# Kernel tuning notes

Hardware: AMD Instinct MI355X
Metric: run time of the kernel (lower is better)

The kernel has to match this reference:

```python
import jax, jax.numpy as jnp
import numpy as np

DIM = 768      # d_model
D_INNER = 768  # int(ssm_ratio * dim)
KK = 16        # K (scan groups)
CD = 48        # Cdim per group (hardcoded self.C)
NS = 16        # d_state
BATCH, SEQ = 8, 4096


def setup_inputs() -> dict:
    key = jax.random.key(0)
    ks = jax.random.split(key, 12)
    s_in = (2.0 / (DIM + 2 * D_INNER)) ** 0.5   # ~xavier
    s_out = (2.0 / (D_INNER + DIM)) ** 0.5
    return {
        "x": jax.random.normal(ks[0], (BATCH, SEQ, DIM), jnp.float32),
        "in_proj_w": jax.random.normal(ks[1], (2 * D_INNER, DIM), jnp.float32) * s_in,
        "in_proj_b": jnp.zeros((2 * D_INNER,), jnp.float32),
        "conv_w": jax.random.normal(ks[2], (D_INNER, 1, 3, 3), jnp.float32) * 0.2,
        "conv_b": jnp.zeros((D_INNER,), jnp.float32),
        "out_proj_w": jax.random.normal(ks[3], (DIM, D_INNER), jnp.float32) * s_out,
        "out_proj_b": jnp.zeros((DIM,), jnp.float32),
        "A_logs": jax.random.normal(ks[4], (KK * CD, NS), jnp.float32) * 0.1,
        "delta": jax.random.normal(ks[5], (BATCH, KK * CD, SEQ), jnp.float32),
        "B_t": jax.random.normal(ks[6], (BATCH, KK, NS, SEQ), jnp.float32),
        "C_t": jax.random.normal(ks[7], (BATCH, KK, NS, SEQ), jnp.float32),
        "delta_bias": jax.random.normal(ks[8], (KK * CD,), jnp.float32),
    }


def reference(x, in_proj_w, in_proj_b, conv_w, conv_b, out_proj_w, out_proj_b,
              A_logs, delta, B_t, C_t, delta_bias):
    # in_proj + chunk; z = silu(z) in the original is dead code (never used)
    h = x @ in_proj_w.T + in_proj_b                      # (B,N,2*D)
    u = h[..., :D_INNER]                                  # (B,N,D)
    # depthwise 3x3 conv on a (B,D,N,1) map (width-1 input, pad 1)
    u = u.transpose(0, 2, 1)[..., None]                   # (B,D,N,1)
    u = jax.lax.conv_general_dilated(
        u, conv_w, window_strides=(1, 1), padding=((1, 1), (1, 1)),
        dimension_numbers=("NCHW", "OIHW", "NCHW"),
        feature_group_count=D_INNER)
    u = jax.nn.silu(u[..., 0] + conv_b[None, :, None])    # (B,D,N)

    # selective_scan_torch math (note: NOT a true recurrence in the source):
    #   delta <- softplus(delta + delta_bias)
    #   y[b,d,l] = delta^2 * u * sum_n A[d,n] * B[b,k(d),n,l] * C[b,k(d),n,l]
    d = jax.nn.softplus(delta + delta_bias[None, :, None])  # (B,D,L)
    A = A_logs.reshape(KK, CD, NS)
    s = jnp.einsum("kcn,bknl->bkcl", A, B_t * C_t)           # (B,K,Cd,L)
    s = s.reshape(u.shape[0], D_INNER, u.shape[2])           # (B,D,L)
    y = d * d * u * s                                        # (B,D,L)

    out = y.transpose(0, 2, 1) @ out_proj_w.T + out_proj_b   # (B,N,dim)
    return out
```

## Files before the change

kernel.cpp:

```cpp
#include <hip/hip_runtime.h>
#include <math.h>

#define B_  8
#define S_  4096
#define D_  768
#define K_  16
#define C_  48
#define N_  16
#define M_  (B_*S_)

typedef float  f32x4  __attribute__((ext_vector_type(4)));
typedef __bf16 bf16x8 __attribute__((ext_vector_type(8)));

__device__ __forceinline__ ushort f2bf(float f) {
  uint u = __builtin_bit_cast(uint, f);
  u += 0x7FFFu + ((u >> 16) & 1u);
  return (ushort)(u >> 16);
}
__device__ __forceinline__ float bf2f(ushort h) {
  return __builtin_bit_cast(float, (uint)h << 16);
}

__global__ __launch_bounds__(256)
void cvt_w(const float* __restrict__ w1, const float* __restrict__ w2,
           ushort* __restrict__ o1, ushort* __restrict__ o2) {
  const int i = blockIdx.x * 256 + threadIdx.x;
  const float* src; ushort* dst; int idx;
  if (i < 147456) { src = w1; dst = o1; idx = i; }
  else            { src = w2; dst = o2; idx = i - 147456; }
  float4 v = *reinterpret_cast<const float4*>(src + (size_t)idx * 4);
  ushort4 o;
  o.x = f2bf(v.x); o.y = f2bf(v.y); o.z = f2bf(v.z); o.w = f2bf(v.w);
  *reinterpret_cast<ushort4*>(dst + (size_t)idx * 4) = o;
}

__global__ __launch_bounds__(256)
void gemm1_xf32(const float* __restrict__ X, const ushort* __restrict__ Wb,
                const float* __restrict__ in_b, ushort* __restrict__ u0T)
{
  __shared__ ushort As[128 * 32];
  __shared__ ushort Bs[128 * 32];

  const int lin = blockIdx.x;
  const int swz = (lin & 7) * 192 + (lin >> 3);
  const int bn  = (swz % 6) * 128;
  const int bm  = (swz / 6) * 128;

  const int tid  = threadIdx.x;
  const int wid  = tid >> 6, lane = tid & 63;
  const int wr   = wid >> 1, wc   = wid & 1;
  const int lr   = lane & 15, lg  = lane >> 4;
  const int srow = lane >> 2;
  const int scol = (lane & 3) * 8;
  const int arow = tid >> 2;
  const int acol = (tid & 3) * 8;

  f32x4 acc[4][4];
#pragma unroll
  for (int i = 0; i < 4; ++i)
#pragma unroll
    for (int j = 0; j < 4; ++j) acc[i][j] = (f32x4){0.f, 0.f, 0.f, 0.f};

  for (int k0 = 0; k0 < 768; k0 += 32) {
#pragma unroll
    for (int half = 0; half < 2; ++half) {
      const int row = arow + half * 64;
      const float* xp = X + (size_t)(bm + row) * 768 + k0 + acol;
      f32x4 v0 = *reinterpret_cast<const f32x4*>(xp);
      f32x4 v1 = *reinterpret_cast<const f32x4*>(xp + 4);
      bf16x8 p = {(__bf16)v0[0], (__bf16)v0[1], (__bf16)v0[2], (__bf16)v0[3],
                  (__bf16)v1[0], (__bf16)v1[1], (__bf16)v1[2], (__bf16)v1[3]};
      *reinterpret_cast<bf16x8*>(&As[row * 32 + acol]) = p;
    }
#pragma unroll
    for (int jj = 0; jj < 2; ++jj) {
      const int j = wid * 2 + jj;
      const ushort* gb = Wb + (size_t)(bn + j * 16 + srow) * 768 + k0 + scol;
      __builtin_amdgcn_global_load_lds(
          (const __attribute__((address_space(1))) void*)gb,
          (__attribute__((address_space(3))) void*)(Bs + j * 512), 16, 0, 0);
    }
    __syncthreads();

    bf16x8 af[4], bfr[4];
    const int ab = (wr * 64 + lr) * 32 + lg * 8;
    const int bb = (wc * 64 + lr) * 32 + lg * 8;
#pragma unroll
    for (int mf = 0; mf < 4; ++mf) af[mf]  = *reinterpret_cast<const bf16x8*>(&As[ab + mf * 512]);
#pragma unroll
    for (int nf = 0; nf < 4; ++nf) bfr[nf] = *reinterpret_cast<const bf16x8*>(&Bs[bb + nf * 512]);
#pragma unroll
    for (int mf = 0; mf < 4; ++mf)
#pragma unroll
      for (int nf = 0; nf < 4; ++nf)
        acc[mf][nf] = __builtin_amdgcn_mfma_f32_16x16x32_bf16(af[mf], bfr[nf], acc[mf][nf], 0, 0, 0);
    __syncthreads();
  }

  const int b   = bm >> 12;
  const int l0g = (bm & 4095) + wr * 64;
#pragma unroll
  for (int nf = 0; nf < 4; ++nf) {
    const int cg = bn + wc * 64 + nf * 16 + lr;
    const float bv = in_b[cg];
    ushort* up = u0T + ((size_t)b * 768 + cg) * 4096 + l0g;
#pragma unroll
    for (int mf = 0; mf < 4; ++mf) {
      ushort4 o;
      o.x = f2bf(acc[mf][nf][0] + bv);
      o.y = f2bf(acc[mf][nf][1] + bv);
      o.z = f2bf(acc[mf][nf][2] + bv);
      o.w = f2bf(acc[mf][nf][3] + bv);
      *reinterpret_cast<ushort4*>(up + mf * 16 + lg * 4) = o;
    }
  }
}

#define YSP 70

__global__ __launch_bounds__(256)
void fuse_mid(const ushort* __restrict__ u0T, const float* __restrict__ delta,
              const float* __restrict__ Bt, const float* __restrict__ Ct,
              const float* __restrict__ Alog, const float* __restrict__ convw,
              const float* __restrict__ convb, const float* __restrict__ dbias,
              ushort* __restrict__ yT)
{
  __shared__ float  Gs [N_ * 64];
  __shared__ float  Ak [C_ * N_];
  __shared__ ushort Ys [C_ * YSP];
  __shared__ float  Wk0[C_], Wk1[C_], Wk2[C_], CB[C_], DB[C_];

  const int tid = threadIdx.x;
  const int wid = tid >> 6, lane = tid & 63;
  const int lt = blockIdx.x, k = blockIdx.y, b = blockIdx.z;
  const int l0 = lt * 64;

  for (int idx = tid; idx < N_ * 64; idx += 256) {
    const int n = idx >> 6, dl = idx & 63;
    const size_t gg = (((size_t)b * K_ + k) * N_ + n) * S_ + l0 + dl;
    Gs[idx] = Bt[gg] * Ct[gg];
  }
  for (int idx = tid; idx < C_ * N_; idx += 256)
    Ak[idx] = Alog[(size_t)k * C_ * N_ + idx];
  if (tid < C_) {
    Wk0[tid] = convw[(k * C_ + tid) * 9 + 1];
    Wk1[tid] = convw[(k * C_ + tid) * 9 + 4];
    Wk2[tid] = convw[(k * C_ + tid) * 9 + 7];
    CB [tid] = convb[k * C_ + tid];
    DB [tid] = dbias[k * C_ + tid];
  }
  __syncthreads();

  float g[N_];
#pragma unroll
  for (int n = 0; n < N_; ++n) g[n] = Gs[n * 64 + lane];

  const int  gl = l0 + lane;
  const size_t base = ((size_t)b * D_ + k * C_ + wid) * S_ + gl;
  const float*  dp = delta + base;
  const ushort* up = u0T + base;
  const size_t cs = (size_t)4 * S_;

  const bool edge_lo = (lane == 0);
  const bool edge_hi = (lane == 63);
  const int  hoff    = edge_lo ? -1 : 1;
  const bool h_ok    = (edge_lo && gl > 0) || (edge_hi && gl + 1 < S_);

  float dA = dp[0];
  float uA = bf2f(up[0]);
  float hA = h_ok ? bf2f(up[hoff]) : 0.f;
  float dB = dp[cs];
  float uB = bf2f(up[cs]);
  float hB = h_ok ? bf2f(up[cs + hoff]) : 0.f;

  for (int step = 0; step < 12; ++step) {
    const int c = step * 4 + wid;
    const float dcur = dA, u0v = uA, hv = hA;
    dA = dB; uA = uB; hA = hB;
    if (step < 10) {
      const size_t off = (size_t)(step + 2) * cs;
      dB = dp[off];
      uB = bf2f(up[off]);
      hB = h_ok ? bf2f(up[off + hoff]) : 0.f;
    }

    float a[N_];
#pragma unroll
    for (int n4i = 0; n4i < 4; ++n4i)
      *reinterpret_cast<f32x4*>(&a[n4i * 4]) =
          *reinterpret_cast<const f32x4*>(&Ak[c * N_ + n4i * 4]);

    const float sm = __shfl(u0v, (lane + 63) & 63, 64);
    const float sp = __shfl(u0v, (lane + 1)  & 63, 64);
    const float um  = edge_lo ? hv : sm;
    const float upv = edge_hi ? hv : sp;

    const float dv = dcur + DB[c];
    const float d  = (dv > 15.f) ? dv : __logf(1.f + __expf(dv));

    float xx = fmaf(Wk0[c], um, fmaf(Wk1[c], u0v, fmaf(Wk2[c], upv, CB[c])));
    const float u = xx * __builtin_amdgcn_rcpf(1.f + __expf(-xx));

    float s = 0.f;
#pragma unroll
    for (int n = 0; n < N_; ++n) s = fmaf(a[n], g[n], s);

    Ys[c * YSP + lane] = f2bf(d * d * u * s);
  }
  __syncthreads();

  {
    uint* yTu = reinterpret_cast<uint*>(yT);
    int dl = tid / 24, j = tid - (tid / 24) * 24;
    for (int e = tid; e < 64 * 24; e += 256) {
      const uint lo = Ys[(2 * j    ) * YSP + dl];
      const uint hi = Ys[(2 * j + 1) * YSP + dl];
      yTu[((size_t)b * S_ + l0 + dl) * 384 + k * 24 + j] = lo | (hi << 16);
      dl += 10; j += 16; if (j >= 24) { j -= 24; dl += 1; }
    }
  }
}

__global__ __launch_bounds__(256)
void gemm_mfma_bt(const ushort* __restrict__ A, const ushort* __restrict__ Bm,
                  const float* __restrict__ bias, float* __restrict__ Cc)
{
  __shared__ ushort As[128 * 32];
  __shared__ ushort Bs[128 * 32];

  const int lin = blockIdx.x;
  const int swz = (lin & 7) * 192 + (lin >> 3);
  const int bn  = (swz % 6) * 128;
  const int bm  = (swz / 6) * 128;

  const int tid  = threadIdx.x;
  const int wid  = tid >> 6, lane = tid & 63;
  const int wr   = wid >> 1, wc   = wid & 1;
  const int lr   = lane & 15, lg  = lane >> 4;
  const int srow = lane >> 2;
  const int scol = (lane & 3) * 8;

  f32x4 acc[4][4];
#pragma unroll
  for (int i = 0; i < 4; ++i)
#pragma unroll
    for (int j = 0; j < 4; ++j) acc[i][j] = (f32x4){0.f, 0.f, 0.f, 0.f};

  for (int k0 = 0; k0 < 768; k0 += 32) {
#pragma unroll
    for (int jj = 0; jj < 2; ++jj) {
      const int j = wid * 2 + jj;
      const ushort* ga = A  + (size_t)(bm + j * 16 + srow) * 768 + k0 + scol;
      __builtin_amdgcn_global_load_lds(
          (const __attribute__((address_space(1))) void*)ga,
          (__attribute__((address_space(3))) void*)(As + j * 512), 16, 0, 0);
      const ushort* gb = Bm + (size_t)(bn + j * 16 + srow) * 768 + k0 + scol;
      __builtin_amdgcn_global_load_lds(
          (const __attribute__((address_space(1))) void*)gb,
          (__attribute__((address_space(3))) void*)(Bs + j * 512), 16, 0, 0);
    }
    __syncthreads();

    bf16x8 af[4], bfr[4];
    const int ab = (wr * 64 + lr) * 32 + lg * 8;
    const int bb = (wc * 64 + lr) * 32 + lg * 8;
#pragma unroll
    for (int mf = 0; mf < 4; ++mf) af[mf]  = *reinterpret_cast<const bf16x8*>(&As[ab + mf * 512]);
#pragma unroll
    for (int nf = 0; nf < 4; ++nf) bfr[nf] = *reinterpret_cast<const bf16x8*>(&Bs[bb + nf * 512]);
#pragma unroll
    for (int mf = 0; mf < 4; ++mf)
#pragma unroll
      for (int nf = 0; nf < 4; ++nf)
        acc[mf][nf] = __builtin_amdgcn_mfma_f32_16x16x32_bf16(af[mf], bfr[nf], acc[mf][nf], 0, 0, 0);
    __syncthreads();
  }

#pragma unroll
  for (int nf = 0; nf < 4; ++nf) {
    const int n  = bn + wc * 64 + nf * 16 + lr;
    const float bv = bias[n];
#pragma unroll
    for (int mf = 0; mf < 4; ++mf) {
      const int m0 = bm + wr * 64 + mf * 16 + lg * 4;
#pragma unroll
      for (int r = 0; r < 4; ++r)
        Cc[(size_t)(m0 + r) * 768 + n] = acc[mf][nf][r] + bv;
    }
  }
}

extern "C" void kernel_launch(void* const* d_in, const int* in_sizes, int n_in,
                              void* d_out, int out_size, void* d_ws, size_t ws_size,
                              hipStream_t stream) {
  const float* x      = (const float*)d_in[0];
  const float* in_w   = (const float*)d_in[1];
  const float* in_b   = (const float*)d_in[2];
  const float* convw  = (const float*)d_in[3];
  const float* convb  = (const float*)d_in[4];
  const float* out_w  = (const float*)d_in[5];
  const float* out_b  = (const float*)d_in[6];
  const float* Alog   = (const float*)d_in[7];
  const float* delta  = (const float*)d_in[8];
  const float* Bt     = (const float*)d_in[9];
  const float* Ct     = (const float*)d_in[10];
  const float* dbias  = (const float*)d_in[11];
  float* out = (float*)d_out;

  ushort* u0T = (ushort*)d_ws;
  ushort* yTb = u0T + (size_t)M_ * D_;
  ushort* wb1 = yTb + (size_t)M_ * D_;
  ushort* wb2 = wb1 + (size_t)D_ * D_;

  cvt_w<<<1152, 256, 0, stream>>>(in_w, out_w, wb1, wb2);
  gemm1_xf32<<<1536, 256, 0, stream>>>(x, wb1, in_b, u0T);
  fuse_mid<<<dim3(S_ / 64, K_, B_), 256, 0, stream>>>(u0T, delta, Bt, Ct, Alog,
                                                      convw, convb, dbias, yTb);
  gemm_mfma_bt<<<1536, 256, 0, stream>>>(yTb, wb2, out_b, out);
}
```

Before: 237.9 us.

## Load GEMM fragments directly from global into registers with prefetch, dropping LDS

```diff
diff --git a/kernel.cpp b/kernel.cpp
--- a/kernel.cpp
+++ b/kernel.cpp
@@ -35,12 +35,9 @@
 }
 
 __global__ __launch_bounds__(256)
-void gemm1_xf32(const float* __restrict__ X, const ushort* __restrict__ Wb,
-                const float* __restrict__ in_b, ushort* __restrict__ u0T)
+void gemm1_direct(const float* __restrict__ X, const ushort* __restrict__ Wb,
+                  const float* __restrict__ in_b, ushort* __restrict__ u0T)
 {
-  __shared__ ushort As[128 * 32];
-  __shared__ ushort Bs[128 * 32];
-
   const int lin = blockIdx.x;
   const int swz = (lin & 7) * 192 + (lin >> 3);
   const int bn  = (swz % 6) * 128;
@@ -50,10 +47,10 @@
   const int wid  = tid >> 6, lane = tid & 63;
   const int wr   = wid >> 1, wc   = wid & 1;
   const int lr   = lane & 15, lg  = lane >> 4;
-  const int srow = lane >> 2;
-  const int scol = (lane & 3) * 8;
-  const int arow = tid >> 2;
-  const int acol = (tid & 3) * 8;
+
+  const float*  xb = X  + (size_t)(bm + wr * 64 + lr) * 768 + lg * 8;
+  const ushort* wb = Wb + (size_t)(bn + wc * 64 + lr) * 768 + lg * 8;
+  const int fs = 16 * 768;
 
   f32x4 acc[4][4];
 #pragma unroll
@@ -61,40 +58,43 @@
 #pragma unroll
     for (int j = 0; j < 4; ++j) acc[i][j] = (f32x4){0.f, 0.f, 0.f, 0.f};
 
+  f32x4  pa0[4], pa1[4];
+  bf16x8 pb[4];
+#pragma unroll
+  for (int mf = 0; mf < 4; ++mf) {
+    pa0[mf] = *reinterpret_cast<const f32x4*>(xb + mf * fs);
+    pa1[mf] = *reinterpret_cast<const f32x4*>(xb + mf * fs + 4);
+  }
+#pragma unroll
+  for (int nf = 0; nf < 4; ++nf)
+    pb[nf] = *reinterpret_cast<const bf16x8*>(wb + nf * fs);
+
   for (int k0 = 0; k0 < 768; k0 += 32) {
-#pragma unroll
-    for (int half = 0; half < 2; ++half) {
-      const int row = arow + half * 64;
-      const float* xp = X + (size_t)(bm + row) * 768 + k0 + acol;
-      f32x4 v0 = *reinterpret_cast<const f32x4*>(xp);
-      f32x4 v1 = *reinterpret_cast<const f32x4*>(xp + 4);
-      bf16x8 p = {(__bf16)v0[0], (__bf16)v0[1], (__bf16)v0[2], (__bf16)v0[3],
-                  (__bf16)v1[0], (__bf16)v1[1], (__bf16)v1[2], (__bf16)v1[3]};
-      *reinterpret_cast<bf16x8*>(&As[row * 32 + acol]) = p;
-    }
-#pragma unroll
-    for (int jj = 0; jj < 2; ++jj) {
-      const int j = wid * 2 + jj;
-      const ushort* gb = Wb + (size_t)(bn + j * 16 + srow) * 768 + k0 + scol;
-      __builtin_amdgcn_global_load_lds(
-          (const __attribute__((address_space(1))) void*)gb,
-          (__attribute__((address_space(3))) void*)(Bs + j * 512), 16, 0, 0);
-    }
-    __syncthreads();
-
-    bf16x8 af[4], bfr[4];
-    const int ab = (wr * 64 + lr) * 32 + lg * 8;
-    const int bb = (wc * 64 + lr) * 32 + lg * 8;
-#pragma unroll
-    for (int mf = 0; mf < 4; ++mf) af[mf]  = *reinterpret_cast<const bf16x8*>(&As[ab + mf * 512]);
-#pragma unroll
-    for (int nf = 0; nf < 4; ++nf) bfr[nf] = *reinterpret_cast<const bf16x8*>(&Bs[bb + nf * 512]);
+    bf16x8 ca[4], cb[4];
 #pragma unroll
     for (int mf = 0; mf < 4; ++mf)
+      ca[mf] = (bf16x8){(__bf16)pa0[mf][0], (__bf16)pa0[mf][1], (__bf16)pa0[mf][2], (__bf16)pa0[mf][3],
+                        (__bf16)pa1[mf][0], (__bf16)pa1[mf][1], (__bf16)pa1[mf][2], (__bf16)pa1[mf][3]};
+#pragma unroll
+    for (int nf = 0; nf < 4; ++nf) cb[nf] = pb[nf];
+
+    if (k0 + 32 < 768) {
+      const int kn = k0 + 32;
+#pragma unroll
+      for (int mf = 0; mf < 4; ++mf) {
+        pa0[mf] = *reinterpret_cast<const f32x4*>(xb + mf * fs + kn);
+        pa1[mf] = *reinterpret_cast<const f32x4*>(xb + mf * fs + kn + 4);
+      }
 #pragma unroll
       for (int nf = 0; nf < 4; ++nf)
-        acc[mf][nf] = __builtin_amdgcn_mfma_f32_16x16x32_bf16(af[mf], bfr[nf], acc[mf][nf], 0, 0, 0);
-    __syncthreads();
+        pb[nf] = *reinterpret_cast<const bf16x8*>(wb + nf * fs + kn);
+    }
+
+#pragma unroll
+    for (int mf = 0; mf < 4; ++mf)
+#pragma unroll
+      for (int nf = 0; nf < 4; ++nf)
+        acc[mf][nf] = __builtin_amdgcn_mfma_f32_16x16x32_bf16(ca[mf], cb[nf], acc[mf][nf], 0, 0, 0);
   }
 
   const int b   = bm >> 12;
@@ -112,6 +112,72 @@
       o.z = f2bf(acc[mf][nf][2] + bv);
       o.w = f2bf(acc[mf][nf][3] + bv);
       *reinterpret_cast<ushort4*>(up + mf * 16 + lg * 4) = o;
+    }
+  }
+}
+
+__global__ __launch_bounds__(256)
+void gemm2_direct(const ushort* __restrict__ A, const ushort* __restrict__ Bm,
+                  const float* __restrict__ bias, float* __restrict__ Cc)
+{
+  const int lin = blockIdx.x;
+  const int swz = (lin & 7) * 192 + (lin >> 3);
+  const int bn  = (swz % 6) * 128;
+  const int bm  = (swz / 6) * 128;
+
+  const int tid  = threadIdx.x;
+  const int wid  = tid >> 6, lane = tid & 63;
+  const int wr   = wid >> 1, wc   = wid & 1;
+  const int lr   = lane & 15, lg  = lane >> 4;
+
+  const ushort* ab = A  + (size_t)(bm + wr * 64 + lr) * 768 + lg * 8;
+  const ushort* wb = Bm + (size_t)(bn + wc * 64 + lr) * 768 + lg * 8;
+  const int fs = 16 * 768;
+
+  f32x4 acc[4][4];
+#pragma unroll
+  for (int i = 0; i < 4; ++i)
+#pragma unroll
+    for (int j = 0; j < 4; ++j) acc[i][j] = (f32x4){0.f, 0.f, 0.f, 0.f};
+
+  bf16x8 pa[4], pb[4];
+#pragma unroll
+  for (int mf = 0; mf < 4; ++mf) pa[mf] = *reinterpret_cast<const bf16x8*>(ab + mf * fs);
+#pragma unroll
+  for (int nf = 0; nf < 4; ++nf) pb[nf] = *reinterpret_cast<const bf16x8*>(wb + nf * fs);
+
+  for (int k0 = 0; k0 < 768; k0 += 32) {
+    bf16x8 ca[4], cb[4];
+#pragma unroll
+    for (int mf = 0; mf < 4; ++mf) ca[mf] = pa[mf];
+#pragma unroll
+    for (int nf = 0; nf < 4; ++nf) cb[nf] = pb[nf];
+
+    if (k0 + 32 < 768) {
+      const int kn = k0 + 32;
+#pragma unroll
+      for (int mf = 0; mf < 4; ++mf) pa[mf] = *reinterpret_cast<const bf16x8*>(ab + mf * fs + kn);
+#pragma unroll
+      for (int nf = 0; nf < 4; ++nf) pb[nf] = *reinterpret_cast<const bf16x8*>(wb + nf * fs + kn);
+    }
+
+#pragma unroll
+    for (int mf = 0; mf < 4; ++mf)
+#pragma unroll
+      for (int nf = 0; nf < 4; ++nf)
+        acc[mf][nf] = __builtin_amdgcn_mfma_f32_16x16x32_bf16(ca[mf], cb[nf], acc[mf][nf], 0, 0, 0);
+  }
+
+#pragma unroll
+  for (int nf = 0; nf < 4; ++nf) {
+    const int n  = bn + wc * 64 + nf * 16 + lr;
+    const float bv = bias[n];
+#pragma unroll
+    for (int mf = 0; mf < 4; ++mf) {
+      const int m0 = bm + wr * 64 + mf * 16 + lg * 4;
+#pragma unroll
+      for (int r = 0; r < 4; ++r)
+        Cc[(size_t)(m0 + r) * 768 + n] = acc[mf][nf][r] + bv;
     }
   }
 }
@@ -217,75 +283,6 @@
       const uint hi = Ys[(2 * j + 1) * YSP + dl];
       yTu[((size_t)b * S_ + l0 + dl) * 384 + k * 24 + j] = lo | (hi << 16);
       dl += 10; j += 16; if (j >= 24) { j -= 24; dl += 1; }
-    }
-  }
-}
-
-__global__ __launch_bounds__(256)
-void gemm_mfma_bt(const ushort* __restrict__ A, const ushort* __restrict__ Bm,
-                  const float* __restrict__ bias, float* __restrict__ Cc)
-{
-  __shared__ ushort As[128 * 32];
-  __shared__ ushort Bs[128 * 32];
-
-  const int lin = blockIdx.x;
-  const int swz = (lin & 7) * 192 + (lin >> 3);
-  const int bn  = (swz % 6) * 128;
-  const int bm  = (swz / 6) * 128;
-
-  const int tid  = threadIdx.x;
-  const int wid  = tid >> 6, lane = tid & 63;
-  const int wr   = wid >> 1, wc   = wid & 1;
-  const int lr   = lane & 15, lg  = lane >> 4;
-  const int srow = lane >> 2;
-  const int scol = (lane & 3) * 8;
-
-  f32x4 acc[4][4];
-#pragma unroll
-  for (int i = 0; i < 4; ++i)
-#pragma unroll
-    for (int j = 0; j < 4; ++j) acc[i][j] = (f32x4){0.f, 0.f, 0.f, 0.f};
-
-  for (int k0 = 0; k0 < 768; k0 += 32) {
-#pragma unroll
-    for (int jj = 0; jj < 2; ++jj) {
-      const int j = wid * 2 + jj;
-      const ushort* ga = A  + (size_t)(bm + j * 16 + srow) * 768 + k0 + scol;
-      __builtin_amdgcn_global_load_lds(
-          (const __attribute__((address_space(1))) void*)ga,
-          (__attribute__((address_space(3))) void*)(As + j * 512), 16, 0, 0);
-      const ushort* gb = Bm + (size_t)(bn + j * 16 + srow) * 768 + k0 + scol;
-      __builtin_amdgcn_global_load_lds(
-          (const __attribute__((address_space(1))) void*)gb,
-          (__attribute__((address_space(3))) void*)(Bs + j * 512), 16, 0, 0);
-    }
-    __syncthreads();
-
-    bf16x8 af[4], bfr[4];
-    const int ab = (wr * 64 + lr) * 32 + lg * 8;
-    const int bb = (wc * 64 + lr) * 32 + lg * 8;
-#pragma unroll
-    for (int mf = 0; mf < 4; ++mf) af[mf]  = *reinterpret_cast<const bf16x8*>(&As[ab + mf * 512]);
-#pragma unroll
-    for (int nf = 0; nf < 4; ++nf) bfr[nf] = *reinterpret_cast<const bf16x8*>(&Bs[bb + nf * 512]);
-#pragma unroll
-    for (int mf = 0; mf < 4; ++mf)
-#pragma unroll
-      for (int nf = 0; nf < 4; ++nf)
-        acc[mf][nf] = __builtin_amdgcn_mfma_f32_16x16x32_bf16(af[mf], bfr[nf], acc[mf][nf], 0, 0, 0);
-    __syncthreads();
-  }
-
-#pragma unroll
-  for (int nf = 0; nf < 4; ++nf) {
-    const int n  = bn + wc * 64 + nf * 16 + lr;
-    const float bv = bias[n];
-#pragma unroll
-    for (int mf = 0; mf < 4; ++mf) {
-      const int m0 = bm + wr * 64 + mf * 16 + lg * 4;
-#pragma unroll
-      for (int r = 0; r < 4; ++r)
-        Cc[(size_t)(m0 + r) * 768 + n] = acc[mf][nf][r] + bv;
     }
   }
 }
@@ -313,8 +310,8 @@
   ushort* wb2 = wb1 + (size_t)D_ * D_;
 
   cvt_w<<<1152, 256, 0, stream>>>(in_w, out_w, wb1, wb2);
-  gemm1_xf32<<<1536, 256, 0, stream>>>(x, wb1, in_b, u0T);
+  gemm1_direct<<<1536, 256, 0, stream>>>(x, wb1, in_b, u0T);
   fuse_mid<<<dim3(S_ / 64, K_, B_), 256, 0, stream>>>(u0T, delta, Bt, Ct, Alog,
                                                       convw, convb, dbias, yTb);
-  gemm_mfma_bt<<<1536, 256, 0, stream>>>(yTb, wb2, out_b, out);
-}
+  gemm2_direct<<<1536, 256, 0, stream>>>(yTb, wb2, out_b, out);
+}
```

New measurement: 427.5 us. 1.8x slower.
